# Kernel tuning notes

Measured on AMD Instinct MI355X. Metric: run time of the kernel, lower is better.

The kernel has to match this reference:

```python
import jax, jax.numpy as jnp
import numpy as np
import math

DIM = 1024
HEADS = 16
PAIR_DIM = 64
POOL = 4  # seq_len // pair_len = 2048 // 512


def central_mask_features(P, feature_size=64):
    half = feature_size // 2
    rel_pos = jnp.arange(2 * P - 1) - (P - 1)                       # [2P-1]
    # torch.logspace(0, log10(P - half + 1), half) == 10**linspace
    widths = jnp.arange(half) + 10.0 ** jnp.linspace(0.0, math.log10(P - half + 1), half)
    emb = (widths[None, :] > rel_pos[:, None]).astype(jnp.float32)  # [2P-1, half]
    signed = jnp.sign(rel_pos)[:, None].astype(jnp.float32) * emb
    return jnp.concatenate([emb, signed], axis=-1)                  # [2P-1, 64]


def relative_shift(x):
    # Faithful replication of the torch pad/view/slice sequence.
    B, P, L, H = x.shape  # L == 2P-1
    x = jnp.pad(x, ((0, 0), (1, 0), (0, 0), (0, 0)))  # [B, P+1, L, H]
    x = x.reshape(B, P + 1, L, H)[:, 1:]              # [B, P, L, H]
    return x[:, :, :P]                                # [B, P, P, H]


def setup_inputs() -> dict:
    key = jax.random.key(0)
    ks = jax.random.split(key, 12)
    HC = HEADS * PAIR_DIM
    s = lambda n: 1.0 / math.sqrt(n)
    return {
        "x": jax.random.normal(ks[0], (4, 2048, DIM), dtype=jnp.float32),
        "Wq": jax.random.normal(ks[1], (HC, DIM), dtype=jnp.float32) * s(DIM),
        "Wk": jax.random.normal(ks[2], (HC, DIM), dtype=jnp.float32) * s(DIM),
        "Wpos": jax.random.normal(ks[3], (HC, 64), dtype=jnp.float32) * s(64),
        "bpos": jax.random.normal(ks[4], (HC,), dtype=jnp.float32) * 0.01,
        "q_bias": jnp.zeros((1, 1, HEADS, PAIR_DIM), dtype=jnp.float32),
        "k_bias": jnp.zeros((1, 1, HEADS, PAIR_DIM), dtype=jnp.float32),
        "Wout": jax.random.normal(ks[5], (PAIR_DIM, HEADS), dtype=jnp.float32) * s(HEADS),
        "bout": jax.random.normal(ks[6], (PAIR_DIM,), dtype=jnp.float32) * 0.01,
        "Wyq": jax.random.normal(ks[7], (PAIR_DIM, DIM), dtype=jnp.float32) * s(DIM),
        "Wyk": jax.random.normal(ks[8], (PAIR_DIM, DIM), dtype=jnp.float32) * s(DIM),
    }


def reference(x, Wq, Wk, Wpos, bpos, q_bias, k_bias, Wout, bout, Wyq, Wyk):
    B, S, D = x.shape
    # AvgPool1d(kernel=stride=POOL) over the sequence dim
    x_ds = x.reshape(B, S // POOL, POOL, D).mean(axis=2)   # [B, P, D]
    P = x_ds.shape[1]
    q = (x_ds @ Wq.T).reshape(B, P, HEADS, PAIR_DIM)
    k = (x_ds @ Wk.T).reshape(B, P, HEADS, PAIR_DIM)
    pos_feat = central_mask_features(P, 64)                 # [2P-1, 64]
    pos_enc = (pos_feat @ Wpos.T + bpos).reshape(2 * P - 1, HEADS, PAIR_DIM)
    rel_q_a = relative_shift(jnp.einsum('bqhc,phc->bqph', q + q_bias, pos_enc))
    rel_k_a = relative_shift(jnp.einsum('bkhc,phc->bkph', k + k_bias, pos_enc))
    dot = jnp.einsum('bqhc,bkhc->bqkh', q, k)               # [B, P, P, H]
    a = dot + (rel_q_a + jnp.transpose(rel_k_a, (0, 2, 1, 3))) * 0.5
    g = jax.nn.gelu(x_ds, approximate=False)                # torch F.gelu exact
    yq = g @ Wyq.T                                          # [B, P, PAIR_DIM]
    yk = g @ Wyk.T
    pair = a @ Wout.T + bout + yq[:, :, None, :] + yk[:, None, :, :]
    return pair                                             # [B, P, P, PAIR_DIM]
```

## Files before the change

kernel.cpp:

```cpp
#include <hip/hip_runtime.h>
#include <math.h>


typedef unsigned short u16;
typedef unsigned int   u32;
typedef __attribute__((ext_vector_type(8)))  short short8;
typedef __attribute__((ext_vector_type(16))) float float16;

#define SEQ 2048
#define DIMN 1024

__device__ __forceinline__ u16 f2bf(float f) {
    union { float f; u32 u; } v; v.f = f;
    u32 r = v.u + 0x7fffu + ((v.u >> 16) & 1u);
    return (u16)(r >> 16);
}
__device__ __forceinline__ float bf2f(u16 h) {
    union { u32 u; float f; } v; v.u = ((u32)h) << 16;
    return v.f;
}
__device__ __forceinline__ void ld_g2l16(u16* lds, const u16* g) {
    __builtin_amdgcn_global_load_lds((const __attribute__((address_space(1))) u32*)g,
                                     (__attribute__((address_space(3))) u32*)lds, 16, 0, 0);
}

struct alignas(8) us4 { u16 x, y, z, w; };

__global__ __launch_bounds__(256) void k_prep(
    const float* __restrict__ x,
    const float* __restrict__ Wq, const float* __restrict__ Wk,
    const float* __restrict__ Wyq, const float* __restrict__ Wyk,
    const float* __restrict__ Wpos, const float* __restrict__ bpos,
    u16* __restrict__ xds, u16* __restrict__ g,
    u16* __restrict__ wqb, u16* __restrict__ wkb,
    u16* __restrict__ wyqb, u16* __restrict__ wykb,
    float* __restrict__ peA, float* __restrict__ peD)
{
    int bk = blockIdx.x, tid = threadIdx.x;
    if (bk < 1024) {
        int i = (bk * 256 + tid) * 4;
        float4 a = *(const float4*)(Wq + i);
        us4 o; o.x=f2bf(a.x); o.y=f2bf(a.y); o.z=f2bf(a.z); o.w=f2bf(a.w);
        *(us4*)(wqb + i) = o;
        a = *(const float4*)(Wk + i);
        o.x=f2bf(a.x); o.y=f2bf(a.y); o.z=f2bf(a.z); o.w=f2bf(a.w);
        *(us4*)(wkb + i) = o;
        if (i < 65536) {
            a = *(const float4*)(Wyq + i);
            o.x=f2bf(a.x); o.y=f2bf(a.y); o.z=f2bf(a.z); o.w=f2bf(a.w);
            *(us4*)(wyqb + i) = o;
            a = *(const float4*)(Wyk + i);
            o.x=f2bf(a.x); o.y=f2bf(a.y); o.z=f2bf(a.z); o.w=f2bf(a.w);
            *(us4*)(wykb + i) = o;
        }
    } else if (bk < 3072) {
        int r = bk - 1024;
        int d4 = tid * 4;
        int b = r >> 9, p = r & 511;
        const float* base = x + ((size_t)(b * SEQ + p * 4)) * DIMN + d4;
        float4 a0 = *(const float4*)(base);
        float4 a1 = *(const float4*)(base + DIMN);
        float4 a2 = *(const float4*)(base + 2 * DIMN);
        float4 a3 = *(const float4*)(base + 3 * DIMN);
        float m0=(a0.x+a1.x+a2.x+a3.x)*0.25f, m1=(a0.y+a1.y+a2.y+a3.y)*0.25f;
        float m2=(a0.z+a1.z+a2.z+a3.z)*0.25f, m3=(a0.w+a1.w+a2.w+a3.w)*0.25f;
        size_t o = (size_t)r * DIMN + d4;
        us4 xo; xo.x=f2bf(m0); xo.y=f2bf(m1); xo.z=f2bf(m2); xo.w=f2bf(m3);
        *(us4*)(xds + o) = xo;
        const float is2 = 0.70710678118654752f;
        us4 go;
        go.x = f2bf(0.5f*m0*(1.f+erff(m0*is2)));
        go.y = f2bf(0.5f*m1*(1.f+erff(m1*is2)));
        go.z = f2bf(0.5f*m2*(1.f+erff(m2*is2)));
        go.w = f2bf(0.5f*m3*(1.f+erff(m3*is2)));
        *(us4*)(g + o) = go;
    } else {
        int t = (bk - 3072) * 256 + tid;
        if (t < 1024) {
            const float* wr = Wpos + t * 64;
            float s1 = 0.f, s2 = 0.f;
            for (int m = 0; m < 32; m++)  s1 += wr[m];
            for (int m = 32; m < 64; m++) s2 += wr[m];
            peA[t] = s1 - s2 + bpos[t];
            peD[t] = s2;
        }
    }
}

__global__ __launch_bounds__(256) void k_gemm(
    const u16* __restrict__ xds, const u16* __restrict__ g,
    const u16* __restrict__ wqb, const u16* __restrict__ wkb,
    const u16* __restrict__ wyqb, const u16* __restrict__ wykb,
    u16* __restrict__ qA, u16* __restrict__ kB,
    float* __restrict__ yqlin, float* __restrict__ yklin)
{
    __shared__ alignas(16) u16 Al[128 * 32];
    __shared__ alignas(16) u16 B0l[64 * 32];
    __shared__ alignas(16) u16 B1l[64 * 32];
    int nt = blockIdx.x, mt = blockIdx.y;
    const u16 *Asrc, *W0, *W1; int col0; int mode;
    if (nt < 16) { Asrc = xds; W0 = wqb;  W1 = wkb;  col0 = nt * 64; mode = 0; }
    else         { Asrc = g;   W0 = wyqb; W1 = wykb; col0 = 0;       mode = 1; }
    int r0 = mt * 128;
    int tid = threadIdx.x;
    int wv = tid >> 6, ln = tid & 63;
    int lane31 = ln & 31, half = ln >> 5;
    float16 aq0, aq1, ak0, ak1;
#pragma unroll
    for (int e = 0; e < 16; e++) { aq0[e]=0.f; aq1[e]=0.f; ak0[e]=0.f; ak1[e]=0.f; }
    int row_l = wv * 32 + lane31;
    int swzA = (row_l >> 1) & 3;
    int colL0 = lane31, colL1 = 32 + lane31;
    int swzB0 = (colL0 >> 1) & 3, swzB1 = (colL1 >> 1) & 3;

    for (int k0 = 0; k0 < 1024; k0 += 32) {
#pragma unroll
        for (int q = 0; q < 2; q++) {
            int n = q * 256 + wv * 64 + ln;
            int row = n >> 2, ccs = n & 3;
            int cc = ccs ^ ((row >> 1) & 3);
            ld_g2l16(Al + (size_t)(q * 256 + wv * 64) * 8,
                     Asrc + (size_t)(r0 + row) * 1024 + k0 + cc * 8);
        }
        {
            int n = wv * 64 + ln;
            int row = n >> 2, ccs = n & 3;
            int cc = ccs ^ ((row >> 1) & 3);
            ld_g2l16(B0l + (size_t)(wv * 64) * 8,
                     W0 + (size_t)(col0 + row) * 1024 + k0 + cc * 8);
            ld_g2l16(B1l + (size_t)(wv * 64) * 8,
                     W1 + (size_t)(col0 + row) * 1024 + k0 + cc * 8);
        }
        __syncthreads();
        short8 a0  = *(const short8*)(Al + (row_l * 4 + ((0 + half) ^ swzA)) * 8);
        short8 a1  = *(const short8*)(Al + (row_l * 4 + ((2 + half) ^ swzA)) * 8);
        short8 q00 = *(const short8*)(B0l + (colL0 * 4 + ((0 + half) ^ swzB0)) * 8);
        short8 q01 = *(const short8*)(B0l + (colL0 * 4 + ((2 + half) ^ swzB0)) * 8);
        short8 q10 = *(const short8*)(B0l + (colL1 * 4 + ((0 + half) ^ swzB1)) * 8);
        short8 q11 = *(const short8*)(B0l + (colL1 * 4 + ((2 + half) ^ swzB1)) * 8);
        short8 k00 = *(const short8*)(B1l + (colL0 * 4 + ((0 + half) ^ swzB0)) * 8);
        short8 k01 = *(const short8*)(B1l + (colL0 * 4 + ((2 + half) ^ swzB0)) * 8);
        short8 k10 = *(const short8*)(B1l + (colL1 * 4 + ((0 + half) ^ swzB1)) * 8);
        short8 k11 = *(const short8*)(B1l + (colL1 * 4 + ((2 + half) ^ swzB1)) * 8);
        aq0 = __builtin_amdgcn_mfma_f32_32x32x16_bf16(a0, q00, aq0, 0, 0, 0);
        aq0 = __builtin_amdgcn_mfma_f32_32x32x16_bf16(a1, q01, aq0, 0, 0, 0);
        aq1 = __builtin_amdgcn_mfma_f32_32x32x16_bf16(a0, q10, aq1, 0, 0, 0);
        aq1 = __builtin_amdgcn_mfma_f32_32x32x16_bf16(a1, q11, aq1, 0, 0, 0);
        ak0 = __builtin_amdgcn_mfma_f32_32x32x16_bf16(a0, k00, ak0, 0, 0, 0);
        ak0 = __builtin_amdgcn_mfma_f32_32x32x16_bf16(a1, k01, ak0, 0, 0, 0);
        ak1 = __builtin_amdgcn_mfma_f32_32x32x16_bf16(a0, k10, ak1, 0, 0, 0);
        ak1 = __builtin_amdgcn_mfma_f32_32x32x16_bf16(a1, k11, ak1, 0, 0, 0);
        __syncthreads();
    }
#pragma unroll
    for (int sel = 0; sel < 4; sel++) {
        int ct = sel & 1;
        bool isq = (sel < 2);
#pragma unroll
        for (int reg = 0; reg < 16; reg++) {
            float v = (sel == 0) ? aq0[reg] : (sel == 1) ? aq1[reg]
                    : (sel == 2) ? ak0[reg] : ak1[reg];
            int rowp = (reg & 3) + 8 * (reg >> 2) + 4 * half;
            int r = r0 + wv * 32 + rowp;
            int col = col0 + ct * 32 + lane31;
            if (mode == 0) {
                int bb = r >> 9, ii = r & 511;
                int h = col >> 6, c = col & 63;
                size_t chunk = ((size_t)((bb * 16 + h) * 8 + (c >> 3))) * 512 + ii;
                u16* dst = isq ? qA : kB;
                dst[chunk * 8 + (c & 7)] = f2bf(v);
            } else {
                float* dst = isq ? yqlin : yklin;
                dst[(size_t)r * 64 + col] = v;
            }
        }
    }
}

__global__ __launch_bounds__(64) void k_uv(
    const u16* __restrict__ qA, const u16* __restrict__ kB,
    const float* __restrict__ yqlin, const float* __restrict__ yklin,
    const float* __restrict__ peA, const float* __restrict__ peD,
    const float* __restrict__ qbias, const float* __restrict__ kbias,
    const float* __restrict__ Wout, const float* __restrict__ bout,
    float* __restrict__ U, float* __restrict__ V,
    float* __restrict__ dU, float* __restrict__ dV)
{
    __shared__ float qrow[1024], krow[1024];
    __shared__ float RA[4][16];
    int r = blockIdx.x; int b = r >> 9, i = r & 511;
    int t = threadIdx.x;
#pragma unroll
    for (int u = 0; u < 2; u++) {
        int cidx = t * 2 + u;
        int h = cidx >> 3, sub = cidx & 7;
        size_t chunk = ((size_t)((b * 16 + h) * 8 + sub)) * 512 + i;
        const u16* sq = qA + chunk * 8;
        const u16* sk = kB + chunk * 8;
        int c0 = h * 64 + sub * 8;
#pragma unroll
        for (int e = 0; e < 8; e++) { qrow[c0 + e] = bf2f(sq[e]); krow[c0 + e] = bf2f(sk[e]); }
    }
    __syncthreads();
    {
        int h = t & 15, which = t >> 4;
        const float* rw = (which < 2) ? qrow : krow;
        const float* bs = (which < 2) ? qbias : kbias;
        const float* pe = (which & 1) ? peD : peA;
        float s = 0.f;
        for (int c = 0; c < 64; c++) s += (rw[h * 64 + c] + bs[h * 64 + c]) * pe[h * 64 + c];
        RA[which][h] = s;
    }
    __syncthreads();
    int d = t;
    float uA = 0.f, uD = 0.f, vA = 0.f, vD = 0.f;
#pragma unroll
    for (int hh = 0; hh < 16; hh++) {
        float w = Wout[d * 16 + hh];
        uA += RA[0][hh] * w; uD += RA[1][hh] * w;
        vA += RA[2][hh] * w; vD += RA[3][hh] * w;
    }
    size_t o = (size_t)r * 64 + d;
    U[o]  = yqlin[o] + 0.5f * uA + bout[d];
    dU[o] = 0.5f * uD;
    V[o]  = yklin[o] + 0.5f * vA;
    dV[o] = 0.5f * vD;
}

__global__ __launch_bounds__(256) void k_main(
    const u16* __restrict__ qA, const u16* __restrict__ kB,
    const float* __restrict__ Wout,
    const float* __restrict__ U, const float* __restrict__ V,
    const float* __restrict__ dU, const float* __restrict__ dV,
    float* __restrict__ out)
{
    __shared__ alignas(16) u16 Asm[1024 * 20];
    int jt = blockIdx.x, it = blockIdx.y, b = blockIdx.z;
    int i0 = it * 32, j0 = jt * 32;
    int tid = threadIdx.x, wv = tid >> 6, ln = tid & 63;
    int lane31 = ln & 31, half = ln >> 5;

    float16 acc[4];
#pragma unroll
    for (int hh = 0; hh < 4; hh++) {
        int h = wv * 4 + hh;
        size_t hbase = ((size_t)(b * 16 + h)) * 8;
        short8 qa[4], kb4[4];
#pragma unroll
        for (int ks = 0; ks < 4; ks++) {
            size_t ch = (hbase + ks * 2 + half) * 512;
            qa[ks]  = *(const short8*)(qA + (ch + i0 + lane31) * 8);
            kb4[ks] = *(const short8*)(kB + (ch + j0 + lane31) * 8);
        }
        float16 a;
#pragma unroll
        for (int e = 0; e < 16; e++) a[e] = 0.f;
#pragma unroll
        for (int ks = 0; ks < 4; ks++)
            a = __builtin_amdgcn_mfma_f32_32x32x16_bf16(qa[ks], kb4[ks], a, 0, 0, 0);
        acc[hh] = a;
    }
#pragma unroll
    for (int reg = 0; reg < 16; reg++) {
        int row = (reg & 3) + 8 * (reg >> 2) + 4 * half;
        int pos = row * 32 + lane31;
        u32 pk0 = (u32)f2bf(acc[0][reg]) | ((u32)f2bf(acc[1][reg]) << 16);
        u32 pk1 = (u32)f2bf(acc[2][reg]) | ((u32)f2bf(acc[3][reg]) << 16);
        u32* bp = (u32*)(Asm + pos * 20 + wv * 4);
        bp[0] = pk0; bp[1] = pk1;
    }
    short8 wfr[2];
#pragma unroll
    for (int dt = 0; dt < 2; dt++) {
        const float* wp = Wout + (dt * 32 + lane31) * 16 + half * 8;
        float4 w0 = *(const float4*)(wp);
        float4 w1 = *(const float4*)(wp + 4);
        short8 t8;
        t8[0]=(short)f2bf(w0.x); t8[1]=(short)f2bf(w0.y); t8[2]=(short)f2bf(w0.z); t8[3]=(short)f2bf(w0.w);
        t8[4]=(short)f2bf(w1.x); t8[5]=(short)f2bf(w1.y); t8[6]=(short)f2bf(w1.z); t8[7]=(short)f2bf(w1.w);
        wfr[dt] = t8;
    }
    float vreg[2][16];
#pragma unroll
    for (int dt = 0; dt < 2; dt++)
#pragma unroll
        for (int reg = 0; reg < 16; reg++) {
            int row = (reg & 3) + 8 * (reg >> 2) + 4 * half;
            vreg[dt][reg] = V[((size_t)(b * 512 + j0 + row)) * 64 + dt * 32 + lane31];
        }
    __syncthreads();
    bool ej_blk = (jt == 15);
    for (int m = 0; m < 8; m++) {
        int il = wv * 8 + m;
        const u16* ap = Asm + (il * 32 + lane31) * 20 + half * 8;
        union { short8 v; uint2 q[2]; } au;
        au.q[0] = *(const uint2*)(ap);
        au.q[1] = *(const uint2*)(ap + 4);
        int ig = i0 + il;
        bool ei = (it == 15) && (il == 31);
        size_t rowbase = (size_t)(b * 512 + ig);
        size_t jbase = (size_t)(b * 512 + j0);
#pragma unroll
        for (int dt = 0; dt < 2; dt++) {
            int dcol = dt * 32 + lane31;
            float16 z;
#pragma unroll
            for (int e = 0; e < 16; e++) z[e] = 0.f;
            float16 pa = __builtin_amdgcn_mfma_f32_32x32x16_bf16(au.v, wfr[dt], z, 0, 0, 0);
            float uval = U[rowbase * 64 + dcol];
            float duv = 0.f;
            if (ej_blk && half) duv = dU[rowbase * 64 + dcol];
            float* ob = out + (rowbase * 512 + j0) * 64 + dcol;
#pragma unroll
            for (int reg = 0; reg < 16; reg++) {
                int row = (reg & 3) + 8 * (reg >> 2) + 4 * half;
                float v = pa[reg] + uval + vreg[dt][reg];
                if (ei) v += dV[(jbase + row) * 64 + dcol];
                if (reg == 15) v += duv;
                __builtin_nontemporal_store(v, ob + (size_t)row * 64);
            }
        }
    }
}

extern "C" void kernel_launch(void* const* d_in, const int* in_sizes, int n_in,
                              void* d_out, int out_size, void* d_ws, size_t ws_size,
                              hipStream_t stream)
{
    const float* x    = (const float*)d_in[0];
    const float* Wq   = (const float*)d_in[1];
    const float* Wk   = (const float*)d_in[2];
    const float* Wpos = (const float*)d_in[3];
    const float* bpos = (const float*)d_in[4];
    const float* qb   = (const float*)d_in[5];
    const float* kb   = (const float*)d_in[6];
    const float* Wout = (const float*)d_in[7];
    const float* bout = (const float*)d_in[8];
    const float* Wyq  = (const float*)d_in[9];
    const float* Wyk  = (const float*)d_in[10];
    float* out = (float*)d_out;
    char* w = (char*)d_ws;
    u16* xds   = (u16*)(w + 0);
    u16* g     = (u16*)(w + 4194304);
    u16* wqb   = (u16*)(w + 8388608);
    u16* wkb   = (u16*)(w + 10485760);
    u16* wyqb  = (u16*)(w + 12582912);
    u16* wykb  = (u16*)(w + 12713984);
    u16* qA    = (u16*)(w + 12845056);
    u16* kB2   = (u16*)(w + 17039360);
    float* yqlin = (float*)(w + 21233664);
    float* yklin = (float*)(w + 21757952);
    float* peA   = (float*)(w + 22282240);
    float* peD   = (float*)(w + 22286336);
    float* U     = (float*)(w + 22290432);
    float* V     = (float*)(w + 22814720);
    float* dU    = (float*)(w + 23339008);
    float* dV    = (float*)(w + 23863296);

    k_prep<<<dim3(3076), dim3(256), 0, stream>>>(x, Wq, Wk, Wyq, Wyk, Wpos, bpos,
                                                 xds, g, wqb, wkb, wyqb, wykb, peA, peD);
    k_gemm<<<dim3(17, 16), dim3(256), 0, stream>>>(xds, g, wqb, wkb, wyqb, wykb,
                                                   qA, kB2, yqlin, yklin);
    k_uv<<<dim3(2048), dim3(64), 0, stream>>>(qA, kB2, yqlin, yklin, peA, peD,
                                              qb, kb, Wout, bout, U, V, dU, dV);
    k_main<<<dim3(16, 16, 4), dim3(256), 0, stream>>>(qA, kB2, Wout, U, V, dU, dV, out);
}
```

Measured before the change: 375.3 us.

## Fold the yq/yk gelu projection into the q/k GEMM blocks

Removes the separate 17th column of blocks that computed the yq/yk projections from gelu(x). Each of the 16 q/k blocks now also loads the gelu tile and an 8-row slice of the Wyq/Wyk weights, and computes a 32x32 MFMA whose first 8 columns hold its share of yq/yk. This spreads the formerly serialized tail work evenly across blocks and avoids load imbalance. The cost is doubled A-tile loads per block (extra LDS and bandwidth) and wasted MFMA columns.

```diff
diff --git a/kernel.cpp b/kernel.cpp
--- a/kernel.cpp
+++ b/kernel.cpp
@@ -95,23 +95,27 @@
     float* __restrict__ yqlin, float* __restrict__ yklin)
 {
     __shared__ alignas(16) u16 Al[128 * 32];
+    __shared__ alignas(16) u16 A2l[128 * 32];
     __shared__ alignas(16) u16 B0l[64 * 32];
     __shared__ alignas(16) u16 B1l[64 * 32];
+    __shared__ alignas(16) u16 B2l[32 * 32];
     int nt = blockIdx.x, mt = blockIdx.y;
-    const u16 *Asrc, *W0, *W1; int col0; int mode;
-    if (nt < 16) { Asrc = xds; W0 = wqb;  W1 = wkb;  col0 = nt * 64; mode = 0; }
-    else         { Asrc = g;   W0 = wyqb; W1 = wykb; col0 = 0;       mode = 1; }
+    int col0 = nt * 64;
     int r0 = mt * 128;
     int tid = threadIdx.x;
     int wv = tid >> 6, ln = tid & 63;
     int lane31 = ln & 31, half = ln >> 5;
-    float16 aq0, aq1, ak0, ak1;
-#pragma unroll
-    for (int e = 0; e < 16; e++) { aq0[e]=0.f; aq1[e]=0.f; ak0[e]=0.f; ak1[e]=0.f; }
+    float16 aq0, aq1, ak0, ak1, ay;
+#pragma unroll
+    for (int e = 0; e < 16; e++) { aq0[e]=0.f; aq1[e]=0.f; ak0[e]=0.f; ak1[e]=0.f; ay[e]=0.f; }
     int row_l = wv * 32 + lane31;
     int swzA = (row_l >> 1) & 3;
     int colL0 = lane31, colL1 = 32 + lane31;
     int swzB0 = (colL0 >> 1) & 3, swzB1 = (colL1 >> 1) & 3;
+    int yrow = (ln >> 2) & 7, yccs = ln & 3;
+    int ycc = yccs ^ ((yrow >> 1) & 3);
+    const u16* ysrc = (yrow < 4 ? wyqb + (size_t)(nt * 4 + yrow) * 1024
+                                : wykb + (size_t)(nt * 4 + yrow - 4) * 1024) + ycc * 8;
 
     for (int k0 = 0; k0 < 1024; k0 += 32) {
 #pragma unroll
@@ -120,20 +124,25 @@
             int row = n >> 2, ccs = n & 3;
             int cc = ccs ^ ((row >> 1) & 3);
             ld_g2l16(Al + (size_t)(q * 256 + wv * 64) * 8,
-                     Asrc + (size_t)(r0 + row) * 1024 + k0 + cc * 8);
+                     xds + (size_t)(r0 + row) * 1024 + k0 + cc * 8);
+            ld_g2l16(A2l + (size_t)(q * 256 + wv * 64) * 8,
+                     g + (size_t)(r0 + row) * 1024 + k0 + cc * 8);
         }
         {
             int n = wv * 64 + ln;
             int row = n >> 2, ccs = n & 3;
             int cc = ccs ^ ((row >> 1) & 3);
             ld_g2l16(B0l + (size_t)(wv * 64) * 8,
-                     W0 + (size_t)(col0 + row) * 1024 + k0 + cc * 8);
+                     wqb + (size_t)(col0 + row) * 1024 + k0 + cc * 8);
             ld_g2l16(B1l + (size_t)(wv * 64) * 8,
-                     W1 + (size_t)(col0 + row) * 1024 + k0 + cc * 8);
-        }
+                     wkb + (size_t)(col0 + row) * 1024 + k0 + cc * 8);
+        }
+        if (wv == 0) ld_g2l16(B2l, ysrc + k0);
         __syncthreads();
-        short8 a0  = *(const short8*)(Al + (row_l * 4 + ((0 + half) ^ swzA)) * 8);
-        short8 a1  = *(const short8*)(Al + (row_l * 4 + ((2 + half) ^ swzA)) * 8);
+        short8 a0  = *(const short8*)(Al  + (row_l * 4 + ((0 + half) ^ swzA)) * 8);
+        short8 a1  = *(const short8*)(Al  + (row_l * 4 + ((2 + half) ^ swzA)) * 8);
+        short8 ag0 = *(const short8*)(A2l + (row_l * 4 + ((0 + half) ^ swzA)) * 8);
+        short8 ag1 = *(const short8*)(A2l + (row_l * 4 + ((2 + half) ^ swzA)) * 8);
         short8 q00 = *(const short8*)(B0l + (colL0 * 4 + ((0 + half) ^ swzB0)) * 8);
         short8 q01 = *(const short8*)(B0l + (colL0 * 4 + ((2 + half) ^ swzB0)) * 8);
         short8 q10 = *(const short8*)(B0l + (colL1 * 4 + ((0 + half) ^ swzB1)) * 8);
@@ -142,6 +151,8 @@
         short8 k01 = *(const short8*)(B1l + (colL0 * 4 + ((2 + half) ^ swzB0)) * 8);
         short8 k10 = *(const short8*)(B1l + (colL1 * 4 + ((0 + half) ^ swzB1)) * 8);
         short8 k11 = *(const short8*)(B1l + (colL1 * 4 + ((2 + half) ^ swzB1)) * 8);
+        short8 y0  = *(const short8*)(B2l + (lane31 * 4 + ((0 + half) ^ swzB0)) * 8);
+        short8 y1  = *(const short8*)(B2l + (lane31 * 4 + ((2 + half) ^ swzB0)) * 8);
         aq0 = __builtin_amdgcn_mfma_f32_32x32x16_bf16(a0, q00, aq0, 0, 0, 0);
         aq0 = __builtin_amdgcn_mfma_f32_32x32x16_bf16(a1, q01, aq0, 0, 0, 0);
         aq1 = __builtin_amdgcn_mfma_f32_32x32x16_bf16(a0, q10, aq1, 0, 0, 0);
@@ -150,6 +161,8 @@
         ak0 = __builtin_amdgcn_mfma_f32_32x32x16_bf16(a1, k01, ak0, 0, 0, 0);
         ak1 = __builtin_amdgcn_mfma_f32_32x32x16_bf16(a0, k10, ak1, 0, 0, 0);
         ak1 = __builtin_amdgcn_mfma_f32_32x32x16_bf16(a1, k11, ak1, 0, 0, 0);
+        ay  = __builtin_amdgcn_mfma_f32_32x32x16_bf16(ag0, y0, ay, 0, 0, 0);
+        ay  = __builtin_amdgcn_mfma_f32_32x32x16_bf16(ag1, y1, ay, 0, 0, 0);
         __syncthreads();
     }
 #pragma unroll
@@ -163,16 +176,21 @@
             int rowp = (reg & 3) + 8 * (reg >> 2) + 4 * half;
             int r = r0 + wv * 32 + rowp;
             int col = col0 + ct * 32 + lane31;
-            if (mode == 0) {
-                int bb = r >> 9, ii = r & 511;
-                int h = col >> 6, c = col & 63;
-                size_t chunk = ((size_t)((bb * 16 + h) * 8 + (c >> 3))) * 512 + ii;
-                u16* dst = isq ? qA : kB;
-                dst[chunk * 8 + (c & 7)] = f2bf(v);
-            } else {
-                float* dst = isq ? yqlin : yklin;
-                dst[(size_t)r * 64 + col] = v;
-            }
+            int bb = r >> 9, ii = r & 511;
+            int h = col >> 6, c = col & 63;
+            size_t chunk = ((size_t)((bb * 16 + h) * 8 + (c >> 3))) * 512 + ii;
+            u16* dst = isq ? qA : kB;
+            dst[chunk * 8 + (c & 7)] = f2bf(v);
+        }
+    }
+    if (lane31 < 8) {
+        float* dst = (lane31 < 4) ? yqlin : yklin;
+        int dcol = nt * 4 + (lane31 & 3);
+#pragma unroll
+        for (int reg = 0; reg < 16; reg++) {
+            int rowp = (reg & 3) + 8 * (reg >> 2) + 4 * half;
+            int r = r0 + wv * 32 + rowp;
+            dst[(size_t)r * 64 + dcol] = ay[reg];
         }
     }
 }
@@ -359,7 +377,7 @@
 
     k_prep<<<dim3(3076), dim3(256), 0, stream>>>(x, Wq, Wk, Wyq, Wyk, Wpos, bpos,
                                                  xds, g, wqb, wkb, wyqb, wykb, peA, peD);
-    k_gemm<<<dim3(17, 16), dim3(256), 0, stream>>>(xds, g, wqb, wkb, wyqb, wykb,
+    k_gemm<<<dim3(16, 16), dim3(256), 0, stream>>>(xds, g, wqb, wkb, wyqb, wykb,
                                                    qA, kB2, yqlin, yklin);
     k_uv<<<dim3(2048), dim3(64), 0, stream>>>(qA, kB2, yqlin, yklin, peA, peD,
                                               qb, kb, Wout, bout, U, V, dU, dV);
```

Result: slower. 390.4 us (+4.0%).
